# Kernel tuning notes

Hardware: AMD Instinct MI355X
Metric: run time of the kernel (lower is better)

## Reference

```python
import jax, jax.numpy as jnp
import numpy as np

K = 20
NEG_SLOPE = 0.2
BN_EPS = 1e-5


def knn_idx(x, k):
    # x: (B, C, N) -> neighbor indices (B, N, k) by largest negative sq-distance
    xt = jnp.swapaxes(x, 1, 2)                      # (B, N, C)
    inner = 2.0 * jnp.einsum('bic,bjc->bij', xt, xt)
    sq = jnp.sum(xt * xt, axis=-1)                  # (B, N)
    dist = inner - sq[:, :, None] - sq[:, None, :]  # -||xi-xj||^2
    _, idx = jax.lax.top_k(dist, k)
    return idx


def edge_feature(x, src, idx):
    # x: (B, C, N) centers; src: (B, C, M) gather source; idx: (B, N, k)
    xt = jnp.swapaxes(x, 1, 2)                      # (B, N, C)
    st = jnp.swapaxes(src, 1, 2)                    # (B, M, C)
    b = jnp.arange(xt.shape[0])[:, None, None]
    neigh = st[b, idx]                              # (B, N, k, C)
    center = xt[:, :, None, :]                      # (B, N, 1, C)
    feat = jnp.concatenate(
        [neigh - center, jnp.broadcast_to(center, neigh.shape)], axis=-1)
    return jnp.transpose(feat, (0, 3, 1, 2))        # (B, 2C, N, k)


def conv_bn_lrelu(x, w, gamma, beta):
    # 1x1 conv (no bias) + training-mode BatchNorm2d + LeakyReLU(0.2)
    y = jnp.einsum('oc,bcnk->bonk', w, x)
    mean = jnp.mean(y, axis=(0, 2, 3), keepdims=True)
    var = jnp.var(y, axis=(0, 2, 3), keepdims=True)
    y = (y - mean) * jax.lax.rsqrt(var + BN_EPS)
    y = y * gamma[None, :, None, None] + beta[None, :, None, None]
    return jnp.where(y >= 0, y, NEG_SLOPE * y)


def knn_ia_idx(x, y, k):
    # cosine-similarity KNN from x (B,Cx,N) into y (B,Cy,M), normalize over channels
    xn = x / jnp.maximum(jnp.linalg.norm(x, axis=1, keepdims=True), 1e-12)
    yn = y / jnp.maximum(jnp.linalg.norm(y, axis=1, keepdims=True), 1e-12)
    simi = jnp.einsum('bci,bcj->bij', xn, yn)       # (B, N, M)
    _, idx = jax.lax.top_k(simi, k)
    return idx


def setup_inputs() -> dict:
    key = jax.random.key(0)
    ks = jax.random.split(key, 8)
    B, N, M, EMB = 8, 1024, 1024, 512
    x = jax.random.normal(ks[0], (B, 3, N), dtype=jnp.float32)
    y = jax.random.normal(ks[1], (B, 128, M), dtype=jnp.float32)
    def w(k_, o, c):
        return jax.random.normal(k_, (o, c), dtype=jnp.float32) * (1.0 / np.sqrt(c))
    inp = {
        'x': x, 'y': y,
        'w1': w(ks[2], 64, 6),
        'w2': w(ks[3], 64, 128),
        'w3': w(ks[4], 128, 128),
        'w4': w(ks[5], 256, 256),
        'w5': w(ks[6], EMB, 512),
        'g1': jnp.ones(64), 'b1': jnp.zeros(64),
        'g2': jnp.ones(64), 'b2': jnp.zeros(64),
        'g3': jnp.ones(128), 'b3': jnp.zeros(128),
        'g4': jnp.ones(256), 'b4': jnp.zeros(256),
        'g5': jnp.ones(EMB), 'b5': jnp.zeros(EMB),
    }
    return inp


def reference(x, y, w1, w2, w3, w4, w5, g1, b1, g2, b2, g3, b3, g4, b4, g5, b5):
    # block 1
    h = conv_bn_lrelu(edge_feature(x, x, knn_idx(x, K)), w1, g1, b1)
    x1 = jnp.max(h, axis=-1)                        # (B, 64, N)
    # block 2
    h = conv_bn_lrelu(edge_feature(x1, x1, knn_idx(x1, K)), w2, g2, b2)
    x2 = jnp.max(h, axis=-1)                        # (B, 64, N)
    # block 3
    h = conv_bn_lrelu(edge_feature(x2, x2, knn_idx(x2, K)), w3, g3, b3)
    x3 = jnp.max(h, axis=-1)                        # (B, 128, N)
    # block 4: cross-attention KNN into y (cosine similarity)
    h = conv_bn_lrelu(edge_feature(x3, y, knn_ia_idx(x3, y, K)), w4, g4, b4)
    x4 = jnp.max(h, axis=-1)                        # (B, 256, N)
    # final 1x1 conv + BN + LeakyReLU on concatenated features (512 ch)
    cat = jnp.concatenate([x1, x2, x3, x4], axis=1)  # (B, 512, N)
    out = conv_bn_lrelu(cat[..., None], w5, g5, b5)[..., 0]
    return out                                       # (B, n_emb_dims, N)
```

## Files before the change

### kernel.cpp

```cpp
#include <hip/hip_runtime.h>
#include <hip/hip_bf16.h>

#define KNN 20
#define NEG_SLOPE 0.2f

constexpr int BB = 8;
constexpr int NN = 1024;
constexpr int MM = 1024;

typedef short bf16x8 __attribute__((ext_vector_type(8)));
typedef float f32x4 __attribute__((ext_vector_type(4)));
typedef double f64x4 __attribute__((ext_vector_type(4)));
typedef unsigned long long u64;

__device__ __forceinline__ u64 pack_key64(double d, int j) {
  u64 u = (u64)__double_as_longlong(d);
  u = (u & 0x8000000000000000ULL) ? ~u : (u | 0x8000000000000000ULL);
  return (u & ~(u64)1023) | (u64)(1023 - j);
}

__device__ __forceinline__ void topk20_u64(u64 (&s)[16], int lane, int* op) {
#pragma unroll
  for (int p = 1; p < 16; p <<= 1) {
#pragma unroll
    for (int k = p; k >= 1; k >>= 1) {
#pragma unroll
      for (int j = k % p; j + k < 16; j += 2 * k) {
#pragma unroll
        for (int i = 0; i < k; ++i) {
          int a = j + i, b = j + i + k;
          if (b < 16 && (a / (2 * p)) == (b / (2 * p))) {
            u64 hi = s[a] > s[b] ? s[a] : s[b];
            u64 lo = s[a] > s[b] ? s[b] : s[a];
            s[a] = hi;
            s[b] = lo;
          }
        }
      }
    }
  }
#pragma unroll
  for (int r = 0; r < KNN; ++r) {
    u64 win = s[0];
#pragma unroll
    for (int off = 32; off > 0; off >>= 1) {
      u64 o = __shfl_xor(win, off, 64);
      win = o > win ? o : win;
    }
    if (lane == 0) op[r] = 1023 - (int)(win & (u64)1023);
    if (s[0] == win) {
#pragma unroll
      for (int i = 0; i < 15; ++i) s[i] = s[i + 1];
      s[15] = 0ULL;
    }
  }
}

__global__ void k_probe_mfma(int* __restrict__ rowt, int* __restrict__ colt,
                             int* __restrict__ flag) {
  __shared__ int cnt[256];
  __shared__ int oksh;
  int tid = threadIdx.x;
  if (tid == 0) oksh = 1;
  for (int e = tid; e < 256; e += 64) cnt[e] = 0;
  __syncthreads();
  int lane = tid & 63;
  f64x4 z = {0.0, 0.0, 0.0, 0.0};
  double ai = (double)(lane & 15);
  double p3 = 1.0, p5 = 1.0;
  int kq = lane >> 4;
  for (int t = 0; t < kq; ++t) { p3 *= 3.0; p5 *= 5.0; }
  f64x4 d1 = __builtin_amdgcn_mfma_f64_16x16x4f64(ai, 1.0, z, 0, 0, 0);
  f64x4 d2 = __builtin_amdgcn_mfma_f64_16x16x4f64(1.0, ai, z, 0, 0, 0);
  f64x4 d3 = __builtin_amdgcn_mfma_f64_16x16x4f64(p3, p5, z, 0, 0, 0);
  bool ok = true;
  int ri[4], ci[4];
#pragma unroll
  for (int r = 0; r < 4; ++r) {
    double va = d1[r], vb = d2[r], vp = d3[r];
    int i = (int)(va * 0.25);
    int j = (int)(vb * 0.25);
    bool e_ok = (i >= 0) && (i < 16) && (j >= 0) && (j < 16) &&
                (va == 4.0 * (double)i) && (vb == 4.0 * (double)j) && (vp == 3616.0);
    if (e_ok) {
      atomicAdd(&cnt[i * 16 + j], 1);
    } else {
      ok = false;
      i = 0;
      j = 0;
    }
    ri[r] = i;
    ci[r] = j;
  }
  if (!ok) atomicExch(&oksh, 0);
  __syncthreads();
  bool bij = true;
  for (int e = tid; e < 256; e += 64)
    if (cnt[e] != 1) bij = false;
  if (!bij) atomicExch(&oksh, 0);
  __syncthreads();
#pragma unroll
  for (int r = 0; r < 4; ++r) {
    rowt[lane * 4 + r] = ri[r];
    colt[lane * 4 + r] = ci[r];
  }
  if (tid == 0) *flag = oksh;
}

__global__ __launch_bounds__(256) void k_transpose_d(
    const float* __restrict__ in, double* __restrict__ out, int C, int Np) {
  int total = BB * C * Np;
  for (int t = blockIdx.x * 256 + threadIdx.x; t < total; t += gridDim.x * 256) {
    int c = t % C;
    int n = (t / C) % Np;
    int b = t / (C * Np);
    out[t] = (double)in[((size_t)b * C + c) * Np + n];
  }
}

__global__ __launch_bounds__(256) void k_cvt_bf16(
    const float* __restrict__ in, __hip_bfloat16* __restrict__ out, int n) {
  int i = blockIdx.x * 256 + threadIdx.x;
  if (i < n) out[i] = __float2bfloat16(in[i]);
}

template <int RECIP>
__global__ __launch_bounds__(256) void k_rowsq(
    const double* __restrict__ A, int ld, int C, double* __restrict__ sq) {
  int p = blockIdx.x * 256 + threadIdx.x;
  if (p >= BB * NN) return;
  const double* row = A + (size_t)p * ld;
  double s = 0.0;
  for (int c = 0; c < C; ++c) { double v = row[c]; s += v * v; }
  if (RECIP) {
    sq[p] = 1.0 / fmax(sqrt(s), 1e-12);
  } else {
    sq[p] = s;
  }
}

__global__ __launch_bounds__(256) void k_knn3(
    const double* __restrict__ xs3, const double* __restrict__ sq, int* __restrict__ idx) {
  __shared__ double P[NN * 3];
  int b = blockIdx.x;
  const double* Xb = xs3 + (size_t)b * NN * 3;
  int tid = threadIdx.x;
  for (int t = tid; t < NN * 3; t += 256) P[t] = Xb[t];
  __syncthreads();
  int wave = tid >> 6, lane = tid & 63;
  int i = blockIdx.y * 4 + wave;
  double xi = P[i * 3], yi = P[i * 3 + 1], zi = P[i * 3 + 2];
  double sqi = sq[b * NN + i];
  u64 s[16];
#pragma unroll
  for (int m = 0; m < 16; ++m) {
    int j = m * 64 + lane;
    double d = fma(xi, P[j * 3], 0.0);
    d = fma(yi, P[j * 3 + 1], d);
    d = fma(zi, P[j * 3 + 2], d);
    s[m] = pack_key64(2.0 * d - sqi - sq[b * NN + j], j);
  }
  int* op = idx + ((size_t)b * NN + i) * KNN;
  topk20_u64(s, lane, op);
}

template <int MODE>
__global__ __launch_bounds__(64, 2) void k_gram_u(
    const double* __restrict__ A, int lda, const double* __restrict__ Bm, int ldb,
    const double* __restrict__ sqA, const double* __restrict__ sqB,
    u64* __restrict__ kk, int C, int b0, const int* __restrict__ rowt,
    const int* __restrict__ colt, const int* __restrict__ flag) {
  __shared__ double As[2][8][69];
  __shared__ double Bs[2][8][69];
  int bg = b0 + blockIdx.x;
  int bl = blockIdx.x;
  int j0 = blockIdx.y * 64;
  int i0 = blockIdx.z * 64;
  const double* Ab = A + (size_t)bg * NN * lda;
  const double* Bb = Bm + (size_t)bg * MM * ldb;
  int lane = threadIdx.x;
  if (*flag) {
    int lm = lane & 15, lq = lane >> 4;
    int k8 = lane & 7, r8 = lane >> 3;
    const double* pa = Ab + (size_t)(i0 + r8) * lda + k8;
    const double* pb = Bb + (size_t)(j0 + r8) * ldb + k8;
    f64x4 acc[4][4] = {};
    double ra[8], rb[8];
#pragma unroll
    for (int r = 0; r < 8; ++r) {
      ra[r] = pa[(size_t)(8 * r) * lda];
      rb[r] = pb[(size_t)(8 * r) * ldb];
    }
#pragma unroll
    for (int r = 0; r < 8; ++r) {
      As[0][k8][r8 + 8 * r] = ra[r];
      Bs[0][k8][r8 + 8 * r] = rb[r];
    }
    int nblk = C >> 3;
    for (int cb = 0; cb < nblk; ++cb) {
      int buf = cb & 1;
      bool pf = (cb + 1 < nblk);
      if (pf) {
        int c0 = (cb + 1) << 3;
#pragma unroll
        for (int r = 0; r < 8; ++r) {
          ra[r] = pa[(size_t)(8 * r) * lda + c0];
          rb[r] = pb[(size_t)(8 * r) * ldb + c0];
        }
      }
#pragma unroll
      for (int kc = 0; kc < 2; ++kc) {
        double a_[4], b_[4];
#pragma unroll
        for (int s = 0; s < 4; ++s) {
          a_[s] = As[buf][kc * 4 + lq][s * 16 + lm];
          b_[s] = Bs[buf][kc * 4 + lq][s * 16 + lm];
        }
#pragma unroll
        for (int si = 0; si < 4; ++si)
#pragma unroll
          for (int sj = 0; sj < 4; ++sj)
            acc[si][sj] = __builtin_amdgcn_mfma_f64_16x16x4f64(a_[si], b_[sj],
                                                               acc[si][sj], 0, 0, 0);
      }
      if (pf) {
        int nb = buf ^ 1;
#pragma unroll
        for (int r = 0; r < 8; ++r) {
          As[nb][k8][r8 + 8 * r] = ra[r];
          Bs[nb][k8][r8 + 8 * r] = rb[r];
        }
      }
    }
    int rta[4], cta[4];
#pragma unroll
    for (int r = 0; r < 4; ++r) {
      rta[r] = rowt[lane * 4 + r];
      cta[r] = colt[lane * 4 + r];
    }
#pragma unroll
    for (int si = 0; si < 4; ++si) {
#pragma unroll
      for (int sj = 0; sj < 4; ++sj) {
#pragma unroll
        for (int r = 0; r < 4; ++r) {
          int i = i0 + si * 16 + rta[r];
          int j = j0 + sj * 16 + cta[r];
          double v = acc[si][sj][r];
          if (MODE == 1)
            v = 2.0 * v - sqA[(size_t)bg * NN + i] - sqB[(size_t)bg * MM + j];
          if (MODE == 2) v = v * sqA[(size_t)bg * NN + i] * sqB[(size_t)bg * MM + j];
          kk[((size_t)bl * NN + i) * MM + j] = pack_key64(v, j);
        }
      }
    }
  } else {
    int lr = lane >> 3, lc = lane & 7;
    double acc2[8][8] = {};
    for (int c0 = 0; c0 < C; c0 += 8) {
      if (c0) __syncthreads();
      for (int r = 0; r < 8; ++r) {
        int li = lane + r * 64;
        int row = li >> 3, k = li & 7;
        As[0][k][row] = Ab[(size_t)(i0 + row) * lda + c0 + k];
        Bs[0][k][row] = Bb[(size_t)(j0 + row) * ldb + c0 + k];
      }
      __syncthreads();
#pragma unroll
      for (int k = 0; k < 8; ++k) {
        double a_[8], b_[8];
#pragma unroll
        for (int t = 0; t < 8; ++t) {
          a_[t] = As[0][k][lr * 8 + t];
          b_[t] = Bs[0][k][lc * 8 + t];
        }
#pragma unroll
        for (int ii = 0; ii < 8; ++ii)
#pragma unroll
          for (int jj = 0; jj < 8; ++jj)
            acc2[ii][jj] = fma(a_[ii], b_[jj], acc2[ii][jj]);
      }
    }
    for (int ii = 0; ii < 8; ++ii) {
      int i = i0 + lr * 8 + ii;
      double qa = sqA[(size_t)bg * NN + i];
      for (int jj = 0; jj < 8; ++jj) {
        int j = j0 + lc * 8 + jj;
        double v = acc2[ii][jj];
        if (MODE == 1) v = 2.0 * v - qa - sqB[(size_t)bg * MM + j];
        if (MODE == 2) v = v * qa * sqB[(size_t)bg * MM + j];
        kk[((size_t)bl * NN + i) * MM + j] = pack_key64(v, j);
      }
    }
  }
}

__global__ __launch_bounds__(64, 2) void k_gram_sym(
    const double* __restrict__ A, int lda, const double* __restrict__ sqA,
    u64* __restrict__ kk, int C, int b0, const int* __restrict__ rowt,
    const int* __restrict__ colt, const int* __restrict__ flag) {
  __shared__ double As[2][8][69];
  __shared__ double Bs[2][8][69];
  int bg = b0 + blockIdx.x;
  int bl = blockIdx.x;
  int p = blockIdx.y;
  int r = (int)((sqrtf(8.f * p + 1.f) - 1.f) * 0.5f);
  while ((r + 1) * (r + 2) / 2 <= p) ++r;
  while (r * (r + 1) / 2 > p) --r;
  int cc = p - r * (r + 1) / 2;
  int i0 = r * 64, j0 = cc * 64;
  const double* Ab = A + (size_t)bg * NN * lda;
  int lane = threadIdx.x;
  if (*flag) {
    int lm = lane & 15, lq = lane >> 4;
    int k8 = lane & 7, r8 = lane >> 3;
    const double* pa = Ab + (size_t)(i0 + r8) * lda + k8;
    const double* pb = Ab + (size_t)(j0 + r8) * lda + k8;
    f64x4 acc[4][4] = {};
    double ra[8], rb[8];
#pragma unroll
    for (int r_ = 0; r_ < 8; ++r_) {
      ra[r_] = pa[(size_t)(8 * r_) * lda];
      rb[r_] = pb[(size_t)(8 * r_) * lda];
    }
#pragma unroll
    for (int r_ = 0; r_ < 8; ++r_) {
      As[0][k8][r8 + 8 * r_] = ra[r_];
      Bs[0][k8][r8 + 8 * r_] = rb[r_];
    }
    int nblk = C >> 3;
    for (int cb = 0; cb < nblk; ++cb) {
      int buf = cb & 1;
      bool pf = (cb + 1 < nblk);
      if (pf) {
        int c0 = (cb + 1) << 3;
#pragma unroll
        for (int r_ = 0; r_ < 8; ++r_) {
          ra[r_] = pa[(size_t)(8 * r_) * lda + c0];
          rb[r_] = pb[(size_t)(8 * r_) * lda + c0];
        }
      }
#pragma unroll
      for (int kc = 0; kc < 2; ++kc) {
        double a_[4], b_[4];
#pragma unroll
        for (int s = 0; s < 4; ++s) {
          a_[s] = As[buf][kc * 4 + lq][s * 16 + lm];
          b_[s] = Bs[buf][kc * 4 + lq][s * 16 + lm];
        }
#pragma unroll
        for (int si = 0; si < 4; ++si)
#pragma unroll
          for (int sj = 0; sj < 4; ++sj)
            acc[si][sj] = __builtin_amdgcn_mfma_f64_16x16x4f64(a_[si], b_[sj],
                                                               acc[si][sj], 0, 0, 0);
      }
      if (pf) {
        int nb = buf ^ 1;
#pragma unroll
        for (int r_ = 0; r_ < 8; ++r_) {
          As[nb][k8][r8 + 8 * r_] = ra[r_];
          Bs[nb][k8][r8 + 8 * r_] = rb[r_];
        }
      }
    }
    int rta[4], cta[4];
#pragma unroll
    for (int r_ = 0; r_ < 4; ++r_) {
      rta[r_] = rowt[lane * 4 + r_];
      cta[r_] = colt[lane * 4 + r_];
    }
    bool mir = (i0 != j0);
#pragma unroll
    for (int si = 0; si < 4; ++si) {
#pragma unroll
      for (int sj = 0; sj < 4; ++sj) {
#pragma unroll
        for (int r_ = 0; r_ < 4; ++r_) {
          int i = i0 + si * 16 + rta[r_];
          int j = j0 + sj * 16 + cta[r_];
          double v = 2.0 * acc[si][sj][r_] - sqA[(size_t)bg * NN + i] -
                     sqA[(size_t)bg * NN + j];
          kk[((size_t)bl * NN + i) * MM + j] = pack_key64(v, j);
          if (mir) kk[((size_t)bl * NN + j) * MM + i] = pack_key64(v, i);
        }
      }
    }
  } else {
    int lr = lane >> 3, lc = lane & 7;
    double acc2[8][8] = {};
    for (int c0 = 0; c0 < C; c0 += 8) {
      if (c0) __syncthreads();
      for (int r_ = 0; r_ < 8; ++r_) {
        int li = lane + r_ * 64;
        int row = li >> 3, k = li & 7;
        As[0][k][row] = Ab[(size_t)(i0 + row) * lda + c0 + k];
        Bs[0][k][row] = Ab[(size_t)(j0 + row) * lda + c0 + k];
      }
      __syncthreads();
#pragma unroll
      for (int k = 0; k < 8; ++k) {
        double a_[8], b_[8];
#pragma unroll
        for (int t = 0; t < 8; ++t) {
          a_[t] = As[0][k][lr * 8 + t];
          b_[t] = Bs[0][k][lc * 8 + t];
        }
#pragma unroll
        for (int ii = 0; ii < 8; ++ii)
#pragma unroll
          for (int jj = 0; jj < 8; ++jj)
            acc2[ii][jj] = fma(a_[ii], b_[jj], acc2[ii][jj]);
      }
    }
    bool mir = (i0 != j0);
    for (int ii = 0; ii < 8; ++ii) {
      int i = i0 + lr * 8 + ii;
      double qa = sqA[(size_t)bg * NN + i];
      for (int jj = 0; jj < 8; ++jj) {
        int j = j0 + lc * 8 + jj;
        double v = 2.0 * acc2[ii][jj] - qa - sqA[(size_t)bg * NN + j];
        kk[((size_t)bl * NN + i) * MM + j] = pack_key64(v, j);
        if (mir) kk[((size_t)bl * NN + j) * MM + i] = pack_key64(v, i);
      }
    }
  }
}

__global__ __launch_bounds__(256) void k_topk(const u64* __restrict__ kk,
                                              int* __restrict__ idx, int b0) {
  int wave = threadIdx.x >> 6;
  int lane = threadIdx.x & 63;
  int bl = blockIdx.x;
  int row = blockIdx.y * 4 + wave;
  const u64* rp = kk + ((size_t)bl * NN + row) * MM;
  u64 s[16];
#pragma unroll
  for (int m = 0; m < 16; ++m) s[m] = rp[m * 64 + lane];
  int* op = idx + ((size_t)(b0 + bl) * NN + row) * KNN;
  topk20_u64(s, lane, op);
}

__global__ __launch_bounds__(256) void k_featmm2(
    const double* __restrict__ src0, int ld0, int Np0,
    const double* __restrict__ src1, int ld1,
    const float* __restrict__ w, int CW,
    double* __restrict__ out0, double* __restrict__ out1, int C, int O,
    const int* __restrict__ rowt, const int* __restrict__ colt,
    const int* __restrict__ flag) {
  __shared__ double As[16][68];
  __shared__ double Ws[16][68];
  int nbo = O >> 6;
  int b = blockIdx.x;
  int mode = blockIdx.y >= nbo;
  int o0 = (blockIdx.y - (mode ? nbo : 0)) * 64;
  int j0 = blockIdx.z * 64;
  const double* src = mode ? src1 : src0;
  int lds_ = mode ? ld1 : ld0;
  int Np = mode ? NN : Np0;
  double* out = mode ? out1 : out0;
  int tid = threadIdx.x;
  const double* Sb = src + (size_t)b * Np * lds_;
  if (*flag) {
    int lane = tid & 63, wv = tid >> 6;
    int lm = lane & 15, lq = lane >> 4;
    f64x4 acc[4] = {};
    for (int c0 = 0; c0 < C; c0 += 16) {
      if (c0) __syncthreads();
      for (int r = 0; r < 4; ++r) {
        int li = tid + r * 256;
        int row = li >> 4, k = li & 15;
        int c = c0 + k;
        As[k][row] = (c < C) ? Sb[(size_t)(j0 + row) * lds_ + c] : 0.0;
        double wvv = 0.0;
        if (c < C) {
          const float* wr = w + (size_t)(o0 + row) * CW;
          wvv = (mode == 0) ? (double)wr[c] : ((double)wr[C + c] - (double)wr[c]);
        }
        Ws[k][row] = wvv;
      }
      __syncthreads();
#pragma unroll
      for (int kc = 0; kc < 4; ++kc) {
        double a = As[kc * 4 + lq][wv * 16 + lm];
#pragma unroll
        for (int t = 0; t < 4; ++t) {
          double bb = Ws[kc * 4 + lq][t * 16 + lm];
          acc[t] = __builtin_amdgcn_mfma_f64_16x16x4f64(a, bb, acc[t], 0, 0, 0);
        }
      }
    }
    int rta[4], cta[4];
#pragma unroll
    for (int r = 0; r < 4; ++r) {
      rta[r] = rowt[lane * 4 + r];
      cta[r] = colt[lane * 4 + r];
    }
#pragma unroll
    for (int t = 0; t < 4; ++t) {
#pragma unroll
      for (int r = 0; r < 4; ++r) {
        int j = j0 + wv * 16 + rta[r];
        int o = o0 + t * 16 + cta[r];
        out[((size_t)b * Np + j) * O + o] = acc[t][r];
      }
    }
  } else {
    int tx = tid & 15, ty = tid >> 4;
    double acc[4][4] = {};
    for (int c0 = 0; c0 < C; c0 += 16) {
      if (c0) __syncthreads();
      for (int r = 0; r < 4; ++r) {
        int li = tid + r * 256;
        int row = li >> 4, k = li & 15;
        int c = c0 + k;
        As[k][row] = (c < C) ? Sb[(size_t)(j0 + row) * lds_ + c] : 0.0;
        double wvv = 0.0;
        if (c < C) {
          const float* wr = w + (size_t)(o0 + row) * CW;
          wvv = (mode == 0) ? (double)wr[c] : ((double)wr[C + c] - (double)wr[c]);
        }
        Ws[k][row] = wvv;
      }
      __syncthreads();
#pragma unroll
      for (int k = 0; k < 16; ++k) {
        double a_[4], b_[4];
#pragma unroll
        for (int ii = 0; ii < 4; ++ii) a_[ii] = As[k][ty * 4 + ii];
#pragma unroll
        for (int jj = 0; jj < 4; ++jj) b_[jj] = Ws[k][tx * 4 + jj];
#pragma unroll
        for (int ii = 0; ii < 4; ++ii)
#pragma unroll
          for (int jj = 0; jj < 4; ++jj)
            acc[ii][jj] = fma(a_[ii], b_[jj], acc[ii][jj]);
      }
    }
    for (int ii = 0; ii < 4; ++ii) {
      int j = j0 + ty * 4 + ii;
      double* op = &out[((size_t)b * Np + j) * O + o0 + tx * 4];
      double2 v0, v1;
      v0.x = acc[ii][0];
      v0.y = acc[ii][1];
      v1.x = acc[ii][2];
      v1.y = acc[ii][3];
      *(double2*)op = v0;
      *(double2*)(op + 2) = v1;
    }
  }
}

__global__ __launch_bounds__(64, 2) void k_gemm5_mfma(
    const __hip_bfloat16* __restrict__ cath, const __hip_bfloat16* __restrict__ w5h,
    float* __restrict__ out) {
  int b = blockIdx.x;
  int j0 = blockIdx.y * 64;
  int o0 = blockIdx.z * 64;
  int lane = threadIdx.x;
  int m = lane & 15;
  int quad = lane >> 4;
  const __hip_bfloat16* arow = cath + ((size_t)(b * NN + j0 + m)) * 512 + quad * 8;
  const __hip_bfloat16* brow = w5h + ((size_t)(o0 + m)) * 512 + quad * 8;
  f32x4 acc[4][4] = {};
#pragma unroll
  for (int c0 = 0; c0 < 512; c0 += 32) {
    bf16x8 a[4], bb[4];
#pragma unroll
    for (int s = 0; s < 4; ++s) {
      a[s] = *(const bf16x8*)(arow + (size_t)s * 16 * 512 + c0);
      bb[s] = *(const bf16x8*)(brow + (size_t)s * 16 * 512 + c0);
    }
#pragma unroll
    for (int si = 0; si < 4; ++si)
#pragma unroll
      for (int sj = 0; sj < 4; ++sj)
        acc[si][sj] =
            __builtin_amdgcn_mfma_f32_16x16x32_bf16(a[si], bb[sj], acc[si][sj], 0, 0, 0);
  }
#pragma unroll
  for (int si = 0; si < 4; ++si) {
    float* ob = &out[((size_t)(b * NN + j0 + si * 16 + quad * 4)) * 512 + o0 + m];
#pragma unroll
    for (int sj = 0; sj < 4; ++sj)
#pragma unroll
      for (int r = 0; r < 4; ++r)
        ob[(size_t)r * 512 + sj * 16] = acc[si][sj][r];
  }
}

__global__ __launch_bounds__(256) void k_gather(
    const double* __restrict__ u, const double* __restrict__ t, const int* __restrict__ idx,
    double* __restrict__ stats, double* __restrict__ mx, int O, int srcNp) {
  __shared__ int lidx[16 * KNN];
  __shared__ double rs[256];
  __shared__ double rq[256];
  int b = blockIdx.z;
  int n0 = blockIdx.y * 16;
  int o0 = blockIdx.x * 64;
  int tid = threadIdx.x;
  int lane = tid & 63, nsl = tid >> 6;
  for (int w = tid; w < 16 * KNN; w += 256)
    lidx[w] = idx[((size_t)b * NN + n0) * KNN + w];
  __syncthreads();
  int oo = o0 + lane;
  double s1 = 0.0, s2 = 0.0;
  for (int ns = nsl; ns < 16; ns += 4) {
    size_t row = (size_t)b * NN + n0 + ns;
    double tv = t[row * O + oo];
    double mxv = -INFINITY;
    double a1 = 0.0, a2 = 0.0;
#pragma unroll
    for (int k = 0; k < KNN; ++k) {
      int j = lidx[ns * KNN + k];
      double yv = u[((size_t)b * srcNp + j) * O + oo] + tv;
      mxv = fmax(mxv, yv);
      a1 += yv;
      a2 = fma(yv, yv, a2);
    }
    mx[row * O + oo] = mxv;
    s1 += a1;
    s2 += a2;
  }
  rs[tid] = s1;
  rq[tid] = s2;
  __syncthreads();
  if (tid < 64) {
    s1 = rs[tid] + rs[tid + 64] + rs[tid + 128] + rs[tid + 192];
    s2 = rq[tid] + rq[tid + 64] + rq[tid + 128] + rq[tid + 192];
    atomicAdd(&stats[o0 + tid], s1);
    atomicAdd(&stats[O + o0 + tid], s2);
  }
}

__global__ __launch_bounds__(256) void k_bnapply(
    const double* __restrict__ mx, const double* __restrict__ u, const double* __restrict__ t,
    const int* __restrict__ idx, const double* __restrict__ stats,
    const float* __restrict__ gamma, const float* __restrict__ beta, double cnt,
    double* __restrict__ catd, __hip_bfloat16* __restrict__ cath, int coff, int O,
    int srcNp) {
  __shared__ double scs[256];
  __shared__ double scc[256];
  int tid = threadIdx.x;
  if (tid < O) {
    double mean = stats[tid] / cnt;
    double var = stats[O + tid] / cnt - mean * mean;
    if (var < 0.0) var = 0.0;
    double rstd = 1.0 / sqrt(var + 1e-5);
    double s = (double)gamma[tid] * rstd;
    scs[tid] = s;
    scc[tid] = (double)beta[tid] - mean * s;
  }
  __syncthreads();
  int i = blockIdx.x * 256 + tid;
  int total = BB * NN * O;
  if (i >= total) return;
  int oo = i % O;
  int n = (i / O) % NN;
  int b = i / (O * NN);
  double s = scs[oo], c = scc[oo];
  double v;
  if (s >= 0.0) {
    v = mx[i];
  } else {
    double tv = t[i];
    double mn = INFINITY;
    for (int k = 0; k < KNN; ++k) {
      int j = idx[((size_t)b * NN + n) * KNN + k];
      mn = fmin(mn, u[((size_t)b * srcNp + j) * O + oo] + tv);
    }
    v = mn;
  }
  double a = s * v + c;
  a = (a >= 0.0) ? a : 0.2 * a;
  size_t ci = ((size_t)b * NN + n) * 512 + coff + oo;
  cath[ci] = __float2bfloat16((float)a);
  if (coff < 256) catd[((size_t)b * NN + n) * 256 + coff + oo] = a;
}

__global__ __launch_bounds__(256) void k_stats512(
    const float* __restrict__ y5, double* __restrict__ stats) {
  int b = blockIdx.y;
  int n0 = blockIdx.x * 32;
  int tid = threadIdx.x;
  for (int part = 0; part < 2; ++part) {
    int oo = tid + part * 256;
    float a1 = 0.f, a2 = 0.f;
    for (int ns = 0; ns < 32; ++ns) {
      float v = y5[((size_t)b * NN + n0 + ns) * 512 + oo];
      a1 += v;
      a2 = fmaf(v, v, a2);
    }
    atomicAdd(&stats[oo], (double)a1);
    atomicAdd(&stats[512 + oo], (double)a2);
  }
}

__global__ __launch_bounds__(256) void k_final5b(
    const float* __restrict__ y5, const double* __restrict__ stats,
    const float* __restrict__ g5, const float* __restrict__ b5,
    float* __restrict__ out) {
  __shared__ float tile[64][65];
  __shared__ double scs[64];
  __shared__ double scc[64];
  int b = blockIdx.z;
  int n0 = blockIdx.x * 64;
  int o0 = blockIdx.y * 64;
  int tid = threadIdx.x;
  if (tid < 64) {
    int o = o0 + tid;
    double cnt = (double)(BB * NN);
    double mean = stats[o] / cnt;
    double var = stats[512 + o] / cnt - mean * mean;
    if (var < 0.0) var = 0.0;
    double rstd = 1.0 / sqrt(var + 1e-5);
    double s = (double)g5[o] * rstd;
    scs[tid] = s;
    scc[tid] = (double)b5[o] - mean * s;
  }
  __syncthreads();
  for (int r = 0; r < 16; ++r) {
    int li = tid + r * 256;
    int nl = li >> 6, ol = li & 63;
    float v = y5[((size_t)b * NN + n0 + nl) * 512 + o0 + ol];
    float a = (float)(scs[ol] * (double)v + scc[ol]);
    a = (a >= 0.f) ? a : NEG_SLOPE * a;
    tile[nl][ol] = a;
  }
  __syncthreads();
  for (int r = 0; r < 16; ++r) {
    int li = tid + r * 256;
    int ol = li >> 6, nl = li & 63;
    out[((size_t)b * 512 + o0 + ol) * NN + n0 + nl] = tile[nl][ol];
  }
}

extern "C" void kernel_launch(void* const* d_in, const int* in_sizes, int n_in,
                              void* d_out, int out_size, void* d_ws, size_t ws_size,
                              hipStream_t stream) {
  const float* x = (const float*)d_in[0];
  const float* y = (const float*)d_in[1];
  const float* w1 = (const float*)d_in[2];
  const float* w2 = (const float*)d_in[3];
  const float* w3 = (const float*)d_in[4];
  const float* w4 = (const float*)d_in[5];
  const float* w5 = (const float*)d_in[6];
  const float* g1 = (const float*)d_in[7];
  const float* b1 = (const float*)d_in[8];
  const float* g2 = (const float*)d_in[9];
  const float* b2 = (const float*)d_in[10];
  const float* g3 = (const float*)d_in[11];
  const float* b3 = (const float*)d_in[12];
  const float* g4 = (const float*)d_in[13];
  const float* b4 = (const float*)d_in[14];
  const float* g5 = (const float*)d_in[15];
  const float* b5 = (const float*)d_in[16];

  char* base = (char*)d_ws;
  size_t off = 0;
  auto alloc = [&](size_t bytes) -> char* {
    char* p = base + off;
    off += (bytes + 255) & ~(size_t)255;
    return p;
  };
  double* stAll = (double*)alloc(5 * 1024 * 8);
  double* sq = (double*)alloc((size_t)BB * NN * 8);
  double* rnx = (double*)alloc((size_t)BB * NN * 8);
  double* rny = (double*)alloc((size_t)BB * MM * 8);
  int* idxb = (int*)alloc((size_t)BB * NN * KNN * 4);
  int* rowt = (int*)alloc(256 * 4);
  int* colt = (int*)alloc(256 * 4);
  int* pflag = (int*)alloc(256);
  double* xs3d = (double*)alloc((size_t)BB * NN * 3 * 8);
  double* ysd = (double*)alloc((size_t)BB * MM * 128 * 8);
  double* catd = (double*)alloc((size_t)BB * NN * 256 * 8);
  __hip_bfloat16* cath = (__hip_bfloat16*)alloc((size_t)BB * NN * 512 * 2);
  __hip_bfloat16* w5h = (__hip_bfloat16*)alloc((size_t)512 * 512 * 2);
  double* uu = (double*)alloc((size_t)BB * MM * 256 * 8);
  double* tt = (double*)alloc((size_t)BB * NN * 256 * 8);
  size_t kkBatchBytes = (size_t)NN * MM * 8;
  size_t avail = (ws_size > off) ? (ws_size - off) : 0;
  int CB = (int)(avail / kkBatchBytes);
  if (CB < 1) CB = 1;
  if (CB > BB) CB = BB;
  u64* KK = (u64*)alloc((size_t)CB * kkBatchBytes);
  float* y5 = (float*)uu;
  double* mx = (double*)d_out;
  float* outp = (float*)d_out;

  const double cntE = (double)BB * NN * KNN;

  auto knn = [&](const double* A, int lda, const double* Bm, int ldb,
                 const double* sa, const double* sb, int C, int sym) {
    for (int b0 = 0; b0 < BB; b0 += CB) {
      int cb = (BB - b0 < CB) ? (BB - b0) : CB;
      if (sym) {
        k_gram_sym<<<dim3(cb, 136), 64, 0, stream>>>(A, lda, sa, KK, C, b0, rowt, colt,
                                                     pflag);
      } else {
        dim3 g(cb, MM / 64, NN / 64);
        k_gram_u<2><<<g, 64, 0, stream>>>(A, lda, Bm, ldb, sa, sb, KK, C, b0, rowt,
                                          colt, pflag);
      }
      k_topk<<<dim3(cb, 256), 256, 0, stream>>>(KK, idxb, b0);
    }
  };

  auto edge_layer = [&](const double* ctr, int ldc, const double* src, int ldsrc,
                        int srcNp, const float* w, int CW, const float* g,
                        const float* bb, int C, int O, int coff, double* st) {
    k_featmm2<<<dim3(8, 2 * (O / 64), 16), 256, 0, stream>>>(
        src, ldsrc, srcNp, ctr, ldc, w, CW, uu, tt, C, O, rowt, colt, pflag);
    k_gather<<<dim3(O / 64, NN / 16, BB), 256, 0, stream>>>(uu, tt, idxb, st, mx, O,
                                                            srcNp);
    k_bnapply<<<(BB * NN * O + 255) / 256, 256, 0, stream>>>(
        mx, uu, tt, idxb, st, g, bb, cntE, catd, cath, coff, O, srcNp);
  };

  hipMemsetAsync(stAll, 0, 5 * 1024 * 8, stream);
  k_probe_mfma<<<1, 64, 0, stream>>>(rowt, colt, pflag);
  k_transpose_d<<<96, 256, 0, stream>>>(x, xs3d, 3, NN);
  k_transpose_d<<<2048, 256, 0, stream>>>(y, ysd, 128, MM);
  k_cvt_bf16<<<1024, 256, 0, stream>>>(w5, w5h, 512 * 512);

  k_rowsq<0><<<32, 256, 0, stream>>>(xs3d, 3, 3, sq);
  k_knn3<<<dim3(BB, 256), 256, 0, stream>>>(xs3d, sq, idxb);
  edge_layer(xs3d, 3, xs3d, 3, NN, w1, 6, g1, b1, 3, 64, 0, stAll);

  k_rowsq<0><<<32, 256, 0, stream>>>(catd, 256, 64, sq);
  knn(catd, 256, catd, 256, sq, sq, 64, 1);
  edge_layer(catd, 256, catd, 256, NN, w2, 128, g2, b2, 64, 64, 64, stAll + 1024);

  k_rowsq<0><<<32, 256, 0, stream>>>(catd + 64, 256, 64, sq);
  knn(catd + 64, 256, catd + 64, 256, sq, sq, 64, 1);
  edge_layer(catd + 64, 256, catd + 64, 256, NN, w3, 128, g3, b3, 64, 128, 128,
             stAll + 2048);

  k_rowsq<1><<<32, 256, 0, stream>>>(catd + 128, 256, 128, rnx);
  k_rowsq<1><<<32, 256, 0, stream>>>(ysd, 128, 128, rny);
  knn(catd + 128, 256, ysd, 128, rnx, rny, 128, 0);
  edge_layer(catd + 128, 256, ysd, 128, MM, w4, 256, g4, b4, 128, 256, 256,
             stAll + 3072);

  double* st5 = stAll + 4096;
  k_gemm5_mfma<<<dim3(8, 16, 8), 64, 0, stream>>>(cath, w5h, y5);
  k_stats512<<<dim3(32, 8), 256, 0, stream>>>(y5, st5);
  k_final5b<<<dim3(16, 8, 8), 256, 0, stream>>>(y5, st5, g5, b5, outp);
}
```

Measured before the change: 631.3 us.

## Switch double feature buffers to channel-major layout and drop LDS staging in Gram kernels

```diff
diff --git a/kernel.cpp b/kernel.cpp
--- a/kernel.cpp
+++ b/kernel.cpp
@@ -107,15 +107,10 @@
   if (tid == 0) *flag = oksh;
 }
 
-__global__ __launch_bounds__(256) void k_transpose_d(
-    const float* __restrict__ in, double* __restrict__ out, int C, int Np) {
-  int total = BB * C * Np;
-  for (int t = blockIdx.x * 256 + threadIdx.x; t < total; t += gridDim.x * 256) {
-    int c = t % C;
-    int n = (t / C) % Np;
-    int b = t / (C * Np);
-    out[t] = (double)in[((size_t)b * C + c) * Np + n];
-  }
+__global__ __launch_bounds__(256) void k_cvt_f64(
+    const float* __restrict__ in, double* __restrict__ out, int n) {
+  for (int i = blockIdx.x * 256 + threadIdx.x; i < n; i += gridDim.x * 256)
+    out[i] = (double)in[i];
 }
 
 __global__ __launch_bounds__(256) void k_cvt_bf16(
@@ -126,12 +121,12 @@
 
 template <int RECIP>
 __global__ __launch_bounds__(256) void k_rowsq(
-    const double* __restrict__ A, int ld, int C, double* __restrict__ sq) {
+    const double* __restrict__ A, int bs, int C, double* __restrict__ sq) {
   int p = blockIdx.x * 256 + threadIdx.x;
-  if (p >= BB * NN) return;
-  const double* row = A + (size_t)p * ld;
+  if (p >= BB * 1024) return;
+  const double* base = A + (size_t)(p >> 10) * bs + (p & 1023);
   double s = 0.0;
-  for (int c = 0; c < C; ++c) { double v = row[c]; s += v * v; }
+  for (int c = 0; c < C; ++c) { double v = base[(size_t)c << 10]; s += v * v; }
   if (RECIP) {
     sq[p] = 1.0 / fmax(sqrt(s), 1e-12);
   } else {
@@ -140,24 +135,24 @@
 }
 
 __global__ __launch_bounds__(256) void k_knn3(
-    const double* __restrict__ xs3, const double* __restrict__ sq, int* __restrict__ idx) {
-  __shared__ double P[NN * 3];
+    const double* __restrict__ xs3c, const double* __restrict__ sq, int* __restrict__ idx) {
+  __shared__ double P[3 * NN];
   int b = blockIdx.x;
-  const double* Xb = xs3 + (size_t)b * NN * 3;
+  const double* Xb = xs3c + (size_t)b * 3 * NN;
   int tid = threadIdx.x;
-  for (int t = tid; t < NN * 3; t += 256) P[t] = Xb[t];
+  for (int t = tid; t < 3 * NN; t += 256) P[t] = Xb[t];
   __syncthreads();
   int wave = tid >> 6, lane = tid & 63;
   int i = blockIdx.y * 4 + wave;
-  double xi = P[i * 3], yi = P[i * 3 + 1], zi = P[i * 3 + 2];
+  double xi = P[i], yi = P[1024 + i], zi = P[2048 + i];
   double sqi = sq[b * NN + i];
   u64 s[16];
 #pragma unroll
   for (int m = 0; m < 16; ++m) {
     int j = m * 64 + lane;
-    double d = fma(xi, P[j * 3], 0.0);
-    d = fma(yi, P[j * 3 + 1], d);
-    d = fma(zi, P[j * 3 + 2], d);
+    double d = fma(xi, P[j], 0.0);
+    d = fma(yi, P[1024 + j], d);
+    d = fma(zi, P[2048 + j], d);
     s[m] = pack_key64(2.0 * d - sqi - sq[b * NN + j], j);
   }
   int* op = idx + ((size_t)b * NN + i) * KNN;
@@ -166,69 +161,51 @@
 
 template <int MODE>
 __global__ __launch_bounds__(64, 2) void k_gram_u(
-    const double* __restrict__ A, int lda, const double* __restrict__ Bm, int ldb,
+    const double* __restrict__ A, int bsA, const double* __restrict__ Bm, int bsB,
     const double* __restrict__ sqA, const double* __restrict__ sqB,
     u64* __restrict__ kk, int C, int b0, const int* __restrict__ rowt,
     const int* __restrict__ colt, const int* __restrict__ flag) {
-  __shared__ double As[2][8][69];
-  __shared__ double Bs[2][8][69];
-  int bg = b0 + blockIdx.x;
-  int bl = blockIdx.x;
-  int j0 = blockIdx.y * 64;
-  int i0 = blockIdx.z * 64;
-  const double* Ab = A + (size_t)bg * NN * lda;
-  const double* Bb = Bm + (size_t)bg * MM * ldb;
+  int bl = blockIdx.z;
+  int bg = b0 + bl;
+  int j0 = blockIdx.x * 64;
+  int i0 = blockIdx.y * 64;
+  const double* Ab = A + (size_t)bg * bsA;
+  const double* Bb = Bm + (size_t)bg * bsB;
   int lane = threadIdx.x;
+  int lm = lane & 15, lq = lane >> 4;
   if (*flag) {
-    int lm = lane & 15, lq = lane >> 4;
-    int k8 = lane & 7, r8 = lane >> 3;
-    const double* pa = Ab + (size_t)(i0 + r8) * lda + k8;
-    const double* pb = Bb + (size_t)(j0 + r8) * ldb + k8;
+    const double* pA = Ab + ((size_t)lq << 10) + i0 + lm;
+    const double* pB = Bb + ((size_t)lq << 10) + j0 + lm;
     f64x4 acc[4][4] = {};
-    double ra[8], rb[8];
-#pragma unroll
-    for (int r = 0; r < 8; ++r) {
-      ra[r] = pa[(size_t)(8 * r) * lda];
-      rb[r] = pb[(size_t)(8 * r) * ldb];
-    }
-#pragma unroll
-    for (int r = 0; r < 8; ++r) {
-      As[0][k8][r8 + 8 * r] = ra[r];
-      Bs[0][k8][r8 + 8 * r] = rb[r];
-    }
-    int nblk = C >> 3;
-    for (int cb = 0; cb < nblk; ++cb) {
-      int buf = cb & 1;
-      bool pf = (cb + 1 < nblk);
+    double a_[4], b_[4], an[4], bn[4];
+#pragma unroll
+    for (int s = 0; s < 4; ++s) {
+      a_[s] = pA[s * 16];
+      b_[s] = pB[s * 16];
+    }
+    int nst = C >> 2;
+    for (int st = 0; st < nst; ++st) {
+      bool pf = (st + 1 < nst);
       if (pf) {
-        int c0 = (cb + 1) << 3;
-#pragma unroll
-        for (int r = 0; r < 8; ++r) {
-          ra[r] = pa[(size_t)(8 * r) * lda + c0];
-          rb[r] = pb[(size_t)(8 * r) * ldb + c0];
-        }
-      }
-#pragma unroll
-      for (int kc = 0; kc < 2; ++kc) {
-        double a_[4], b_[4];
+        pA += (size_t)4 << 10;
+        pB += (size_t)4 << 10;
 #pragma unroll
         for (int s = 0; s < 4; ++s) {
-          a_[s] = As[buf][kc * 4 + lq][s * 16 + lm];
-          b_[s] = Bs[buf][kc * 4 + lq][s * 16 + lm];
-        }
-#pragma unroll
-        for (int si = 0; si < 4; ++si)
-#pragma unroll
-          for (int sj = 0; sj < 4; ++sj)
-            acc[si][sj] = __builtin_amdgcn_mfma_f64_16x16x4f64(a_[si], b_[sj],
-                                                               acc[si][sj], 0, 0, 0);
-      }
+          an[s] = pA[s * 16];
+          bn[s] = pB[s * 16];
+        }
+      }
+#pragma unroll
+      for (int si = 0; si < 4; ++si)
+#pragma unroll
+        for (int sj = 0; sj < 4; ++sj)
+          acc[si][sj] =
+              __builtin_amdgcn_mfma_f64_16x16x4f64(a_[si], b_[sj], acc[si][sj], 0, 0, 0);
       if (pf) {
-        int nb = buf ^ 1;
-#pragma unroll
-        for (int r = 0; r < 8; ++r) {
-          As[nb][k8][r8 + 8 * r] = ra[r];
-          Bs[nb][k8][r8 + 8 * r] = rb[r];
+#pragma unroll
+        for (int s = 0; s < 4; ++s) {
+          a_[s] = an[s];
+          b_[s] = bn[s];
         }
       }
     }
@@ -257,29 +234,18 @@
   } else {
     int lr = lane >> 3, lc = lane & 7;
     double acc2[8][8] = {};
-    for (int c0 = 0; c0 < C; c0 += 8) {
-      if (c0) __syncthreads();
-      for (int r = 0; r < 8; ++r) {
-        int li = lane + r * 64;
-        int row = li >> 3, k = li & 7;
-        As[0][k][row] = Ab[(size_t)(i0 + row) * lda + c0 + k];
-        Bs[0][k][row] = Bb[(size_t)(j0 + row) * ldb + c0 + k];
-      }
-      __syncthreads();
-#pragma unroll
-      for (int k = 0; k < 8; ++k) {
-        double a_[8], b_[8];
-#pragma unroll
-        for (int t = 0; t < 8; ++t) {
-          a_[t] = As[0][k][lr * 8 + t];
-          b_[t] = Bs[0][k][lc * 8 + t];
-        }
-#pragma unroll
-        for (int ii = 0; ii < 8; ++ii)
-#pragma unroll
-          for (int jj = 0; jj < 8; ++jj)
-            acc2[ii][jj] = fma(a_[ii], b_[jj], acc2[ii][jj]);
-      }
+    for (int c = 0; c < C; ++c) {
+      double aa[8], bb[8];
+#pragma unroll
+      for (int t = 0; t < 8; ++t) {
+        aa[t] = Ab[((size_t)c << 10) + i0 + lr * 8 + t];
+        bb[t] = Bb[((size_t)c << 10) + j0 + lc * 8 + t];
+      }
+#pragma unroll
+      for (int ii = 0; ii < 8; ++ii)
+#pragma unroll
+        for (int jj = 0; jj < 8; ++jj)
+          acc2[ii][jj] = fma(aa[ii], bb[jj], acc2[ii][jj]);
     }
     for (int ii = 0; ii < 8; ++ii) {
       int i = i0 + lr * 8 + ii;
@@ -296,71 +262,53 @@
 }
 
 __global__ __launch_bounds__(64, 2) void k_gram_sym(
-    const double* __restrict__ A, int lda, const double* __restrict__ sqA,
+    const double* __restrict__ A, int bsA, const double* __restrict__ sqA,
     u64* __restrict__ kk, int C, int b0, const int* __restrict__ rowt,
     const int* __restrict__ colt, const int* __restrict__ flag) {
-  __shared__ double As[2][8][69];
-  __shared__ double Bs[2][8][69];
-  int bg = b0 + blockIdx.x;
-  int bl = blockIdx.x;
-  int p = blockIdx.y;
+  int p = blockIdx.x;
   int r = (int)((sqrtf(8.f * p + 1.f) - 1.f) * 0.5f);
   while ((r + 1) * (r + 2) / 2 <= p) ++r;
   while (r * (r + 1) / 2 > p) --r;
   int cc = p - r * (r + 1) / 2;
   int i0 = r * 64, j0 = cc * 64;
-  const double* Ab = A + (size_t)bg * NN * lda;
+  int bl = blockIdx.y;
+  int bg = b0 + bl;
+  const double* Ab = A + (size_t)bg * bsA;
   int lane = threadIdx.x;
+  int lm = lane & 15, lq = lane >> 4;
   if (*flag) {
-    int lm = lane & 15, lq = lane >> 4;
-    int k8 = lane & 7, r8 = lane >> 3;
-    const double* pa = Ab + (size_t)(i0 + r8) * lda + k8;
-    const double* pb = Ab + (size_t)(j0 + r8) * lda + k8;
+    const double* pA = Ab + ((size_t)lq << 10) + i0 + lm;
+    const double* pB = Ab + ((size_t)lq << 10) + j0 + lm;
     f64x4 acc[4][4] = {};
-    double ra[8], rb[8];
-#pragma unroll
-    for (int r_ = 0; r_ < 8; ++r_) {
-      ra[r_] = pa[(size_t)(8 * r_) * lda];
-      rb[r_] = pb[(size_t)(8 * r_) * lda];
-    }
-#pragma unroll
-    for (int r_ = 0; r_ < 8; ++r_) {
-      As[0][k8][r8 + 8 * r_] = ra[r_];
-      Bs[0][k8][r8 + 8 * r_] = rb[r_];
-    }
-    int nblk = C >> 3;
-    for (int cb = 0; cb < nblk; ++cb) {
-      int buf = cb & 1;
-      bool pf = (cb + 1 < nblk);
+    double a_[4], b_[4], an[4], bn[4];
+#pragma unroll
+    for (int s = 0; s < 4; ++s) {
+      a_[s] = pA[s * 16];
+      b_[s] = pB[s * 16];
+    }
+    int nst = C >> 2;
+    for (int st = 0; st < nst; ++st) {
+      bool pf = (st + 1 < nst);
       if (pf) {
-        int c0 = (cb + 1) << 3;
-#pragma unroll
-        for (int r_ = 0; r_ < 8; ++r_) {
-          ra[r_] = pa[(size_t)(8 * r_) * lda + c0];
-          rb[r_] = pb[(size_t)(8 * r_) * lda + c0];
-        }
-      }
-#pragma unroll
-      for (int kc = 0; kc < 2; ++kc) {
-        double a_[4], b_[4];
+        pA += (size_t)4 << 10;
+        pB += (size_t)4 << 10;
 #pragma unroll
         for (int s = 0; s < 4; ++s) {
-          a_[s] = As[buf][kc * 4 + lq][s * 16 + lm];
-          b_[s] = Bs[buf][kc * 4 + lq][s * 16 + lm];
-        }
-#pragma unroll
-        for (int si = 0; si < 4; ++si)
-#pragma unroll
-          for (int sj = 0; sj < 4; ++sj)
-            acc[si][sj] = __builtin_amdgcn_mfma_f64_16x16x4f64(a_[si], b_[sj],
-                                                               acc[si][sj], 0, 0, 0);
-      }
+          an[s] = pA[s * 16];
+          bn[s] = pB[s * 16];
+        }
+      }
+#pragma unroll
+      for (int si = 0; si < 4; ++si)
+#pragma unroll
+        for (int sj = 0; sj < 4; ++sj)
+          acc[si][sj] =
+              __builtin_amdgcn_mfma_f64_16x16x4f64(a_[si], b_[sj], acc[si][sj], 0, 0, 0);
       if (pf) {
-        int nb = buf ^ 1;
-#pragma unroll
-        for (int r_ = 0; r_ < 8; ++r_) {
-          As[nb][k8][r8 + 8 * r_] = ra[r_];
-          Bs[nb][k8][r8 + 8 * r_] = rb[r_];
+#pragma unroll
+        for (int s = 0; s < 4; ++s) {
+          a_[s] = an[s];
+          b_[s] = bn[s];
         }
       }
     }
@@ -389,29 +337,18 @@
   } else {
     int lr = lane >> 3, lc = lane & 7;
     double acc2[8][8] = {};
-    for (int c0 = 0; c0 < C; c0 += 8) {
-      if (c0) __syncthreads();
-      for (int r_ = 0; r_ < 8; ++r_) {
-        int li = lane + r_ * 64;
-        int row = li >> 3, k = li & 7;
-        As[0][k][row] = Ab[(size_t)(i0 + row) * lda + c0 + k];
-        Bs[0][k][row] = Ab[(size_t)(j0 + row) * lda + c0 + k];
-      }
-      __syncthreads();
-#pragma unroll
-      for (int k = 0; k < 8; ++k) {
-        double a_[8], b_[8];
-#pragma unroll
-        for (int t = 0; t < 8; ++t) {
-          a_[t] = As[0][k][lr * 8 + t];
-          b_[t] = Bs[0][k][lc * 8 + t];
-        }
-#pragma unroll
-        for (int ii = 0; ii < 8; ++ii)
-#pragma unroll
-          for (int jj = 0; jj < 8; ++jj)
-            acc2[ii][jj] = fma(a_[ii], b_[jj], acc2[ii][jj]);
-      }
+    for (int c = 0; c < C; ++c) {
+      double aa[8], bb[8];
+#pragma unroll
+      for (int t = 0; t < 8; ++t) {
+        aa[t] = Ab[((size_t)c << 10) + i0 + lr * 8 + t];
+        bb[t] = Ab[((size_t)c << 10) + j0 + lc * 8 + t];
+      }
+#pragma unroll
+      for (int ii = 0; ii < 8; ++ii)
+#pragma unroll
+        for (int jj = 0; jj < 8; ++jj)
+          acc2[ii][jj] = fma(aa[ii], bb[jj], acc2[ii][jj]);
     }
     bool mir = (i0 != j0);
     for (int ii = 0; ii < 8; ++ii) {
@@ -442,8 +379,8 @@
 }
 
 __global__ __launch_bounds__(256) void k_featmm2(
-    const double* __restrict__ src0, int ld0, int Np0,
-    const double* __restrict__ src1, int ld1,
+    const double* __restrict__ src0, int bs0, int Np0,
+    const double* __restrict__ src1, int bs1,
     const float* __restrict__ w, int CW,
     double* __restrict__ out0, double* __restrict__ out1, int C, int O,
     const int* __restrict__ rowt, const int* __restrict__ colt,
@@ -456,11 +393,11 @@
   int o0 = (blockIdx.y - (mode ? nbo : 0)) * 64;
   int j0 = blockIdx.z * 64;
   const double* src = mode ? src1 : src0;
-  int lds_ = mode ? ld1 : ld0;
+  int bs = mode ? bs1 : bs0;
   int Np = mode ? NN : Np0;
   double* out = mode ? out1 : out0;
   int tid = threadIdx.x;
-  const double* Sb = src + (size_t)b * Np * lds_;
+  const double* Sb = src + (size_t)b * bs;
   if (*flag) {
     int lane = tid & 63, wv = tid >> 6;
     int lm = lane & 15, lq = lane >> 4;
@@ -469,9 +406,11 @@
       if (c0) __syncthreads();
       for (int r = 0; r < 4; ++r) {
         int li = tid + r * 256;
+        int rowA = li & 63, kA = li >> 6;
+        int cA = c0 + kA;
+        As[kA][rowA] = (cA < C) ? Sb[((size_t)cA << 10) + j0 + rowA] : 0.0;
         int row = li >> 4, k = li & 15;
         int c = c0 + k;
-        As[k][row] = (c < C) ? Sb[(size_t)(j0 + row) * lds_ + c] : 0.0;
         double wvv = 0.0;
         if (c < C) {
           const float* wr = w + (size_t)(o0 + row) * CW;
@@ -512,9 +451,11 @@
       if (c0) __syncthreads();
       for (int r = 0; r < 4; ++r) {
         int li = tid + r * 256;
+        int rowA = li & 63, kA = li >> 6;
+        int cA = c0 + kA;
+        As[kA][rowA] = (cA < C) ? Sb[((size_t)cA << 10) + j0 + rowA] : 0.0;
         int row = li >> 4, k = li & 15;
         int c = c0 + k;
-        As[k][row] = (c < C) ? Sb[(size_t)(j0 + row) * lds_ + c] : 0.0;
         double wvv = 0.0;
         if (c < C) {
           const float* wr = w + (size_t)(o0 + row) * CW;
@@ -675,7 +616,8 @@
   a = (a >= 0.0) ? a : 0.2 * a;
   size_t ci = ((size_t)b * NN + n) * 512 + coff + oo;
   cath[ci] = __float2bfloat16((float)a);
-  if (coff < 256) catd[((size_t)b * NN + n) * 256 + coff + oo] = a;
+  if (coff < 256)
+    catd[(size_t)b * 256 * NN + ((size_t)(coff + oo) << 10) + n] = a;
 }
 
 __global__ __launch_bounds__(256) void k_stats512(
@@ -771,9 +713,9 @@
   int* rowt = (int*)alloc(256 * 4);
   int* colt = (int*)alloc(256 * 4);
   int* pflag = (int*)alloc(256);
-  double* xs3d = (double*)alloc((size_t)BB * NN * 3 * 8);
-  double* ysd = (double*)alloc((size_t)BB * MM * 128 * 8);
-  double* catd = (double*)alloc((size_t)BB * NN * 256 * 8);
+  double* xs3c = (double*)alloc((size_t)BB * 3 * NN * 8);
+  double* ysd = (double*)alloc((size_t)BB * 128 * MM * 8);
+  double* catd = (double*)alloc((size_t)BB * 256 * NN * 8);
   __hip_bfloat16* cath = (__hip_bfloat16*)alloc((size_t)BB * NN * 512 * 2);
   __hip_bfloat16* w5h = (__hip_bfloat16*)alloc((size_t)512 * 512 * 2);
   double* uu = (double*)alloc((size_t)BB * MM * 256 * 8);
@@ -790,27 +732,27 @@
 
   const double cntE = (double)BB * NN * KNN;
 
-  auto knn = [&](const double* A, int lda, const double* Bm, int ldb,
+  auto knn = [&](const double* A, int bsA, const double* Bm, int bsB,
                  const double* sa, const double* sb, int C, int sym) {
     for (int b0 = 0; b0 < BB; b0 += CB) {
       int cb = (BB - b0 < CB) ? (BB - b0) : CB;
       if (sym) {
-        k_gram_sym<<<dim3(cb, 136), 64, 0, stream>>>(A, lda, sa, KK, C, b0, rowt, colt,
+        k_gram_sym<<<dim3(136, cb), 64, 0, stream>>>(A, bsA, sa, KK, C, b0, rowt, colt,
                                                      pflag);
       } else {
-        dim3 g(cb, MM / 64, NN / 64);
-        k_gram_u<2><<<g, 64, 0, stream>>>(A, lda, Bm, ldb, sa, sb, KK, C, b0, rowt,
+        dim3 g(MM / 64, NN / 64, cb);
+        k_gram_u<2><<<g, 64, 0, stream>>>(A, bsA, Bm, bsB, sa, sb, KK, C, b0, rowt,
                                           colt, pflag);
       }
       k_topk<<<dim3(cb, 256), 256, 0, stream>>>(KK, idxb, b0);
     }
   };
 
-  auto edge_layer = [&](const double* ctr, int ldc, const double* src, int ldsrc,
+  auto edge_layer = [&](const double* ctr, int bsc, const double* src, int bss,
                         int srcNp, const float* w, int CW, const float* g,
                         const float* bb, int C, int O, int coff, double* st) {
     k_featmm2<<<dim3(8, 2 * (O / 64), 16), 256, 0, stream>>>(
-        src, ldsrc, srcNp, ctr, ldc, w, CW, uu, tt, C, O, rowt, colt, pflag);
+        src, bss, srcNp, ctr, bsc, w, CW, uu, tt, C, O, rowt, colt, pflag);
     k_gather<<<dim3(O / 64, NN / 16, BB), 256, 0, stream>>>(uu, tt, idxb, st, mx, O,
                                                             srcNp);
     k_bnapply<<<(BB * NN * O + 255) / 256, 256, 0, stream>>>(
@@ -819,28 +761,29 @@
 
   hipMemsetAsync(stAll, 0, 5 * 1024 * 8, stream);
   k_probe_mfma<<<1, 64, 0, stream>>>(rowt, colt, pflag);
-  k_transpose_d<<<96, 256, 0, stream>>>(x, xs3d, 3, NN);
-  k_transpose_d<<<2048, 256, 0, stream>>>(y, ysd, 128, MM);
+  k_cvt_f64<<<96, 256, 0, stream>>>(x, xs3c, BB * 3 * NN);
+  k_cvt_f64<<<2048, 256, 0, stream>>>(y, ysd, BB * 128 * MM);
   k_cvt_bf16<<<1024, 256, 0, stream>>>(w5, w5h, 512 * 512);
 
-  k_rowsq<0><<<32, 256, 0, stream>>>(xs3d, 3, 3, sq);
-  k_knn3<<<dim3(BB, 256), 256, 0, stream>>>(xs3d, sq, idxb);
-  edge_layer(xs3d, 3, xs3d, 3, NN, w1, 6, g1, b1, 3, 64, 0, stAll);
-
-  k_rowsq<0><<<32, 256, 0, stream>>>(catd, 256, 64, sq);
-  knn(catd, 256, catd, 256, sq, sq, 64, 1);
-  edge_layer(catd, 256, catd, 256, NN, w2, 128, g2, b2, 64, 64, 64, stAll + 1024);
-
-  k_rowsq<0><<<32, 256, 0, stream>>>(catd + 64, 256, 64, sq);
-  knn(catd + 64, 256, catd + 64, 256, sq, sq, 64, 1);
-  edge_layer(catd + 64, 256, catd + 64, 256, NN, w3, 128, g3, b3, 64, 128, 128,
-             stAll + 2048);
-
-  k_rowsq<1><<<32, 256, 0, stream>>>(catd + 128, 256, 128, rnx);
-  k_rowsq<1><<<32, 256, 0, stream>>>(ysd, 128, 128, rny);
-  knn(catd + 128, 256, ysd, 128, rnx, rny, 128, 0);
-  edge_layer(catd + 128, 256, ysd, 128, MM, w4, 256, g4, b4, 128, 256, 256,
-             stAll + 3072);
+  k_rowsq<0><<<32, 256, 0, stream>>>(xs3c, 3 * NN, 3, sq);
+  k_knn3<<<dim3(BB, 256), 256, 0, stream>>>(xs3c, sq, idxb);
+  edge_layer(xs3c, 3 * NN, xs3c, 3 * NN, NN, w1, 6, g1, b1, 3, 64, 0, stAll);
+
+  k_rowsq<0><<<32, 256, 0, stream>>>(catd, 256 * NN, 64, sq);
+  knn(catd, 256 * NN, catd, 256 * NN, sq, sq, 64, 1);
+  edge_layer(catd, 256 * NN, catd, 256 * NN, NN, w2, 128, g2, b2, 64, 64, 64,
+             stAll + 1024);
+
+  k_rowsq<0><<<32, 256, 0, stream>>>(catd + 64 * NN, 256 * NN, 64, sq);
+  knn(catd + 64 * NN, 256 * NN, catd + 64 * NN, 256 * NN, sq, sq, 64, 1);
+  edge_layer(catd + 64 * NN, 256 * NN, catd + 64 * NN, 256 * NN, NN, w3, 128, g3, b3,
+             64, 128, 128, stAll + 2048);
+
+  k_rowsq<1><<<32, 256, 0, stream>>>(catd + 128 * NN, 256 * NN, 128, rnx);
+  k_rowsq<1><<<32, 256, 0, stream>>>(ysd, 128 * MM, 128, rny);
+  knn(catd + 128 * NN, 256 * NN, ysd, 128 * MM, rnx, rny, 128, 0);
+  edge_layer(catd + 128 * NN, 256 * NN, ysd, 128 * MM, MM, w4, 256, g4, b4, 128, 256,
+             256, stAll + 3072);
 
   double* st5 = stAll + 4096;
   k_gemm5_mfma<<<dim3(8, 16, 8), 64, 0, stream>>>(cath, w5h, y5);
```

Result: slower. 727.3 us (+15.2%).
